# Performance work log

Hardware: AMD Instinct MI355X
Metric: run time of the kernel (lower is better)

Reference implementation:

```python
import jax, jax.numpy as jnp
import numpy as np
import math

# Config mirroring init_kwargs / input_specs
BATCH, N, D_IN, RANK = 8, 2048, 256, 64
TAU = 1.0
TOPK = 32
EDGE_DROPOUT = 0.1
EPS = 1e-6


def setup_inputs() -> dict:
    key = jax.random.key(0)
    k1, k2, k3 = jax.random.split(key, 3)
    X = jax.random.normal(k1, (BATCH, N, D_IN), dtype=jnp.float32)
    W = jax.random.normal(k2, (D_IN, RANK), dtype=jnp.float32) / math.sqrt(D_IN)
    # b_init='identity_perturbed': identity plus small noise
    B = jnp.eye(RANK, dtype=jnp.float32) + 0.01 * jax.random.normal(k3, (RANK, RANK), dtype=jnp.float32)
    return {"X": X, "W": W, "B": B}


def _zero_diag(A):
    n = A.shape[-1]
    return A * (1.0 - jnp.eye(n, dtype=A.dtype))


def _row_normalize(A):
    denom = jnp.clip(jnp.sum(A, axis=-1, keepdims=True), EPS, None)
    return A / denom


def reference(X, W, B):
    # FDG: low-rank node embedding R, bilinear scores S, softmax adjacency A
    R = jnp.einsum('bnd,dr->bnr', X, W)                       # [B, N, rank]
    S = jnp.einsum('bnr,rk,bmk->bnm', R, B, R) / jnp.asarray(math.sqrt(RANK), R.dtype)  # [B, N, N]
    A = jax.nn.softmax(S / TAU, axis=-1)

    # topk_sparsify_adjacency (mask=None)
    scores = _zero_diag(A)
    k = max(1, min(TOPK, N - 1))
    vals, idx = jax.lax.top_k(scores, k)                      # [B, N, k]
    bI = jnp.arange(BATCH)[:, None, None]
    nI = jnp.arange(N)[None, :, None]
    sparse = jnp.zeros_like(scores).at[bI, nI, idx].set(vals)
    A = _row_normalize(sparse)

    # edge_dropout_adjacency (training=True)
    keep_prob = 1.0 - EDGE_DROPOUT
    keep = (jax.random.uniform(jax.random.key(42), A.shape) <= keep_prob).astype(A.dtype)
    A = _zero_diag(A) * keep / max(keep_prob, 1e-6)
    A = _row_normalize(A)
    return (A, S, R)
```

## Files before the change

### kernel.cpp

```cpp
#include <hip/hip_runtime.h>
#include <math.h>

#define BATCH 8
#define NN 2048
#define DIN 256
#define RANK 64
#define TOPKK 32

static constexpr size_t A_ELEMS = (size_t)BATCH * NN * NN;
static constexpr size_t S_OFF   = A_ELEMS;
static constexpr size_t R_OFF   = 2 * A_ELEMS;

#define NEG_INF (-__builtin_inff())

__device__ __forceinline__ unsigned rotl32(unsigned x, int d) {
  return (x << d) | (x >> (32 - d));
}

__device__ unsigned threefry_bits(unsigned flat) {
  const unsigned ks0 = 0u, ks1 = 42u, ks2 = 0u ^ 42u ^ 0x1BD11BDAu;
  unsigned x0 = 0u + ks0;
  unsigned x1 = flat + ks1;
#define TF_ROUND(r) { x0 += x1; x1 = rotl32(x1, r); x1 ^= x0; }
  TF_ROUND(13) TF_ROUND(15) TF_ROUND(26) TF_ROUND(6)
  x0 += ks1; x1 += ks2 + 1u;
  TF_ROUND(17) TF_ROUND(29) TF_ROUND(16) TF_ROUND(24)
  x0 += ks2; x1 += ks0 + 2u;
  TF_ROUND(13) TF_ROUND(15) TF_ROUND(26) TF_ROUND(6)
  x0 += ks0; x1 += ks1 + 3u;
  TF_ROUND(17) TF_ROUND(29) TF_ROUND(16) TF_ROUND(24)
  x0 += ks1; x1 += ks2 + 4u;
  TF_ROUND(13) TF_ROUND(15) TF_ROUND(26) TF_ROUND(6)
  x0 += ks2; x1 += ks0 + 5u;
#undef TF_ROUND
  return x0 ^ x1;
}

__device__ __forceinline__ unsigned long long make_key(float v, int col) {
  unsigned u = __float_as_uint(v);
  u = (u & 0x80000000u) ? ~u : (u | 0x80000000u);
  return ((unsigned long long)u << 32) | (unsigned)(~col);
}

__global__ __launch_bounds__(256) void rt_kernel(const float* __restrict__ X,
                                                 const float* __restrict__ W,
                                                 const float* __restrict__ Bm,
                                                 float* __restrict__ out) {
  __shared__ float Xs[32][256];
  __shared__ float Bs[64][64];
  __shared__ float Rs[32][64];
  const int t = threadIdx.x;
  const int blk = blockIdx.x;
  const int b  = blk >> 6;
  const int rb = blk & 63;
  const float* Xb = X + ((size_t)b * NN + (size_t)rb * 32) * DIN;

#pragma unroll
  for (int it = 0; it < 8; ++it) {
    int flat = it * 1024 + t * 4;
    float4 f = *(const float4*)(Xb + flat);
    *(float4*)&Xs[flat >> 8][flat & 255] = f;
  }
#pragma unroll
  for (int it = 0; it < 4; ++it) {
    int flat = it * 1024 + t * 4;
    float4 f = *(const float4*)(Bm + flat);
    *(float4*)&Bs[flat >> 6][flat & 63] = f;
  }
  __syncthreads();

  const int j = t & 63, rg = t >> 6;
  float acc[8] = {0.f, 0.f, 0.f, 0.f, 0.f, 0.f, 0.f, 0.f};
  for (int k = 0; k < DIN; k += 4) {
    float w0 = W[(k + 0) * RANK + j];
    float w1 = W[(k + 1) * RANK + j];
    float w2 = W[(k + 2) * RANK + j];
    float w3 = W[(k + 3) * RANK + j];
#pragma unroll
    for (int ii = 0; ii < 8; ++ii) {
      float4 xv = *(const float4*)&Xs[rg * 8 + ii][k];
      acc[ii] += xv.x * w0 + xv.y * w1 + xv.z * w2 + xv.w * w3;
    }
  }
  const size_t grow0 = (size_t)b * NN + (size_t)rb * 32;
  float* Rout = out + R_OFF + grow0 * RANK;
#pragma unroll
  for (int ii = 0; ii < 8; ++ii) {
    Rout[(size_t)(rg * 8 + ii) * RANK + j] = acc[ii];
    Rs[rg * 8 + ii][j] = acc[ii];
  }
  __syncthreads();

  float acc2[8] = {0.f, 0.f, 0.f, 0.f, 0.f, 0.f, 0.f, 0.f};
  for (int r = 0; r < RANK; r += 4) {
    float b0 = Bs[r + 0][j];
    float b1 = Bs[r + 1][j];
    float b2 = Bs[r + 2][j];
    float b3 = Bs[r + 3][j];
#pragma unroll
    for (int ii = 0; ii < 8; ++ii) {
      float4 rv = *(const float4*)&Rs[rg * 8 + ii][r];
      acc2[ii] += rv.x * b0 + rv.y * b1 + rv.z * b2 + rv.w * b3;
    }
  }
  float* Tout = out + grow0 * RANK;
#pragma unroll
  for (int ii = 0; ii < 8; ++ii)
    Tout[(size_t)(rg * 8 + ii) * RANK + j] = acc2[ii] * 0.125f;
}

__global__ __launch_bounds__(256) void s_kernel(float* __restrict__ out) {
  __shared__ float Ts[64][68];
  __shared__ float Rs[64][68];
  const int t = threadIdx.x;
  const int bx = blockIdx.x;
  const int by = blockIdx.y;
  const int bz = blockIdx.z;
  const float* Tg = out + ((size_t)bz * NN + (size_t)by * 64) * RANK;
  const float* Rg = out + R_OFF + ((size_t)bz * NN + (size_t)bx * 64) * RANK;

#pragma unroll
  for (int it = 0; it < 4; ++it) {
    int flat = it * 1024 + t * 4;
    int r = flat >> 6, c = flat & 63;
    *(float4*)&Ts[r][c] = *(const float4*)(Tg + flat);
    *(float4*)&Rs[r][c] = *(const float4*)(Rg + flat);
  }
  __syncthreads();

  const int tx = t & 15, ty = t >> 4;
  float acc[4][4];
#pragma unroll
  for (int ii = 0; ii < 4; ++ii)
#pragma unroll
    for (int jj = 0; jj < 4; ++jj) acc[ii][jj] = 0.f;

  for (int k = 0; k < 64; k += 4) {
    float4 a[4], bb[4];
#pragma unroll
    for (int ii = 0; ii < 4; ++ii) a[ii] = *(const float4*)&Ts[ty + 16 * ii][k];
#pragma unroll
    for (int jj = 0; jj < 4; ++jj) bb[jj] = *(const float4*)&Rs[tx + 16 * jj][k];
#pragma unroll
    for (int ii = 0; ii < 4; ++ii)
#pragma unroll
      for (int jj = 0; jj < 4; ++jj)
        acc[ii][jj] += a[ii].x * bb[jj].x + a[ii].y * bb[jj].y +
                       a[ii].z * bb[jj].z + a[ii].w * bb[jj].w;
  }

  float* Sb = out + S_OFF + (size_t)bz * NN * NN;
#pragma unroll
  for (int ii = 0; ii < 4; ++ii) {
    int n = by * 64 + ty + 16 * ii;
#pragma unroll
    for (int jj = 0; jj < 4; ++jj) {
      int m = bx * 64 + tx + 16 * jj;
      Sb[(size_t)n * NN + m] = acc[ii][jj];
    }
  }
}

__global__ __launch_bounds__(64) void topk_kernel(const float* __restrict__ Sg,
                                                  float* __restrict__ A) {
  __shared__ float rowbuf[NN];
  __shared__ unsigned long long keys[64];
  __shared__ int cnt;
  const int lane = threadIdx.x;
  const int wave = blockIdx.x;
  const int n = wave & (NN - 1);

  const float* row = Sg + (size_t)wave * NN;
  float v[32];
#pragma unroll
  for (int jj = 0; jj < 8; ++jj) {
    float4 f = *(const float4*)(row + jj * 256 + lane * 4);
    v[jj * 4 + 0] = f.x; v[jj * 4 + 1] = f.y;
    v[jj * 4 + 2] = f.z; v[jj * 4 + 3] = f.w;
  }

  float s = 0.f, ss = 0.f;
#pragma unroll
  for (int jj = 0; jj < 32; ++jj) { s += v[jj]; ss = fmaf(v[jj], v[jj], ss); }
#pragma unroll
  for (int off = 1; off < 64; off <<= 1) {
    s  += __shfl_xor(s, off, 64);
    ss += __shfl_xor(ss, off, 64);
  }
  const float mu = s * (1.f / 2048.f);
  const float sigma = sqrtf(fmaxf(ss * (1.f / 2048.f) - mu * mu, 1e-12f));

  {
    int d = n - lane * 4;
    if (d >= 0 && d < NN && (d & 255) < 4)
      v[((d >> 8) << 2) | (d & 3)] = NEG_INF;
  }

  float tau = mu + 2.0641f * sigma;
  float lo_b = -3.0e38f, hi_b = 3.0e38f;
  float step = sigma + 1e-20f;
  bool found = false;
  for (int it = 0; it < 40; ++it) {
    int cl = 0;
#pragma unroll
    for (int jj = 0; jj < 32; ++jj) cl += (v[jj] > tau) ? 1 : 0;
#pragma unroll
    for (int off = 1; off < 64; off <<= 1) cl += __shfl_xor(cl, off, 64);
    if (cl >= TOPKK && cl <= 64) { found = true; break; }
    if (cl > 64) lo_b = fmaxf(lo_b, tau); else hi_b = fminf(hi_b, tau);
    float tn = 0.f; bool ok = false;
    if (it < 6) {
      float p = fminf(fmaxf((float)cl, 1.f) * (1.f / 2048.f), 0.5f);
      float tt = sqrtf(-2.f * logf(p));
      float zc = tt - (2.30753f + 0.27061f * tt) /
                      (1.f + tt * (0.99229f + 0.04481f * tt));
      zc = fmaxf(zc, 0.05f);
      tn = mu + 2.0641f * ((tau - mu) / zc);
      ok = (tn > lo_b && tn < hi_b);
    }
    if (!ok) {
      if (lo_b > -1.0e38f && hi_b < 1.0e38f) tn = 0.5f * lo_b + 0.5f * hi_b;
      else if (cl > 64) { tn = tau + step; step *= 2.f; }
      else             { tn = tau - step; step *= 2.f; }
    }
    tau = tn;
  }

  if (lane == 0) cnt = 0;
  __syncthreads();

  if (found) {
#pragma unroll
    for (int jj = 0; jj < 32; ++jj) {
      if (v[jj] > tau) {
        int col = ((jj >> 2) << 8) + lane * 4 + (jj & 3);
        int pos = atomicAdd(&cnt, 1);
        if (pos < 64) keys[pos] = make_key(v[jj], col);
      }
    }
  } else {
    unsigned alive = 0xFFFFFFFFu;
    if (lane == 0) cnt = TOPKK;
    for (int it = 0; it < TOPKK; ++it) {
      unsigned long long best = 0ull;
#pragma unroll
      for (int jj = 0; jj < 32; ++jj) {
        if ((alive >> jj) & 1u) {
          int col = ((jj >> 2) << 8) + lane * 4 + (jj & 3);
          unsigned long long k = make_key(v[jj], col);
          if (k > best) best = k;
        }
      }
      unsigned long long b2 = best;
#pragma unroll
      for (int off = 1; off < 64; off <<= 1) {
        unsigned long long o = __shfl_xor(b2, off, 64);
        if (o > b2) b2 = o;
      }
      if (lane == 0) keys[it] = b2;
      if (best == b2) {
#pragma unroll
        for (int jj = 0; jj < 32; ++jj) {
          int col = ((jj >> 2) << 8) + lane * 4 + (jj & 3);
          if (make_key(v[jj], col) == b2) alive &= ~(1u << jj);
        }
      }
    }
  }
  __syncthreads();

  const int cn = min(cnt, 64);
  unsigned long long key = (lane < cn) ? keys[lane] : 0ull;

#pragma unroll
  for (int k = 2; k <= 64; k <<= 1) {
#pragma unroll
    for (int j = k >> 1; j >= 1; j >>= 1) {
      unsigned long long o = __shfl_xor(key, j, 64);
      bool lower = (lane & j) == 0;
      bool desc  = (lane & k) == 0;
      bool takeMax = (lower == desc);
      bool kgo = key > o;
      key = (takeMax == kgo) ? key : o;
    }
  }

  float val; int col;
  {
    unsigned hi = (unsigned)(key >> 32);
    unsigned ub = (hi & 0x80000000u) ? (hi ^ 0x80000000u) : ~hi;
    val = __uint_as_float(ub);
    col = (int)(~(unsigned)key) & (NN - 1);
  }

  float m = __shfl(val, 0, 64);
  float e = (lane < TOPKK) ? expf(val - m) : 0.f;
  float s1 = e;
#pragma unroll
  for (int off = 1; off < 64; off <<= 1) s1 += __shfl_xor(s1, off, 64);
  float a1 = e / fmaxf(s1, 1e-6f);

  float a2 = 0.f;
  if (lane < TOPKK) {
    unsigned flat = (unsigned)wave * 2048u + (unsigned)col;
    unsigned bits = threefry_bits(flat);
    float u = __uint_as_float((bits >> 9) | 0x3f800000u) - 1.0f;
    if (u <= 0.9f) a2 = a1 * (1.f / 0.9f);
  }
  float s2 = a2;
#pragma unroll
  for (int off = 1; off < 64; off <<= 1) s2 += __shfl_xor(s2, off, 64);
  float av = a2 / fmaxf(s2, 1e-6f);

#pragma unroll
  for (int jj = 0; jj < 8; ++jj)
    *(float4*)&rowbuf[jj * 256 + lane * 4] = make_float4(0.f, 0.f, 0.f, 0.f);
  __syncthreads();
  if (lane < TOPKK) rowbuf[col] = av;
  __syncthreads();
  float* Arow = A + (size_t)wave * NN;
#pragma unroll
  for (int jj = 0; jj < 8; ++jj)
    *(float4*)(Arow + jj * 256 + lane * 4) = *(float4*)&rowbuf[jj * 256 + lane * 4];
}

extern "C" void kernel_launch(void* const* d_in, const int* in_sizes, int n_in,
                              void* d_out, int out_size, void* d_ws, size_t ws_size,
                              hipStream_t stream) {
  const float* X  = (const float*)d_in[0];
  const float* W  = (const float*)d_in[1];
  const float* Bm = (const float*)d_in[2];
  float* out = (float*)d_out;

  hipLaunchKernelGGL(rt_kernel, dim3(512), dim3(256), 0, stream, X, W, Bm, out);
  hipLaunchKernelGGL(s_kernel, dim3(32, 32, 8), dim3(256), 0, stream, out);
  hipLaunchKernelGGL(topk_kernel, dim3(16384), dim3(64), 0, stream, out + S_OFF, out);
}
```

Baseline: 163.7 us.

## Fuse S computation with threshold candidate extraction using analytic row statistics

Computes per-batch Gram matrix R^T R and column sums of R, then derives each row's mean and variance of S analytically to set a top-k threshold before S is formed. The S GEMM kernel now also emits candidate keys above that threshold into a workspace, so the top-k pass mostly sorts a short candidate list instead of rereading and iteratively thresholding the full S row. Rows whose candidate count falls outside the accepted range fall back to the old full-row search. This adds workspace traffic, atomics and two small reduction kernels. The fused kernel uses only 256 blocks of 512 threads, which risks underfilling the GPU.

After: 207.9 us. 27.0% more time.

```diff
diff --git a/kernel.cpp b/kernel.cpp
--- a/kernel.cpp
+++ b/kernel.cpp
@@ -6,10 +6,18 @@
 #define DIN 256
 #define RANK 64
 #define TOPKK 32
+#define CANDMAX 96
 
 static constexpr size_t A_ELEMS = (size_t)BATCH * NN * NN;
 static constexpr size_t S_OFF   = A_ELEMS;
 static constexpr size_t R_OFF   = 2 * A_ELEMS;
+static constexpr size_t NROWS   = (size_t)BATCH * NN;
+
+static constexpr size_t G_OFF      = 0;
+static constexpr size_t U_OFF      = 32768;
+static constexpr size_t GP_OFF     = 33280;
+static constexpr size_t CNT_OFF_F  = GP_OFF + 64 * 4160;
+static constexpr size_t CAND_OFF_F = CNT_OFF_F + NROWS;
 
 #define NEG_INF (-__builtin_inff())
 
@@ -42,6 +50,28 @@
   return ((unsigned long long)u << 32) | (unsigned)(~col);
 }
 
+__device__ __forceinline__ void decode_key(unsigned long long key, float& val, int& col) {
+  unsigned hi = (unsigned)(key >> 32);
+  unsigned ub = (hi & 0x80000000u) ? (hi ^ 0x80000000u) : ~hi;
+  val = __uint_as_float(ub);
+  col = (int)(~(unsigned)key) & (NN - 1);
+}
+
+__device__ __forceinline__ void bitonic64_desc(unsigned long long& key, int lane) {
+#pragma unroll
+  for (int k = 2; k <= 64; k <<= 1) {
+#pragma unroll
+    for (int j = k >> 1; j >= 1; j >>= 1) {
+      unsigned long long o = __shfl_xor(key, j, 64);
+      bool lower = (lane & j) == 0;
+      bool desc  = (lane & k) == 0;
+      bool takeMax = (lower == desc);
+      bool kgo = key > o;
+      key = (takeMax == kgo) ? key : o;
+    }
+  }
+}
+
 __global__ __launch_bounds__(256) void rt_kernel(const float* __restrict__ X,
                                                  const float* __restrict__ W,
                                                  const float* __restrict__ Bm,
@@ -58,14 +88,12 @@
 #pragma unroll
   for (int it = 0; it < 8; ++it) {
     int flat = it * 1024 + t * 4;
-    float4 f = *(const float4*)(Xb + flat);
-    *(float4*)&Xs[flat >> 8][flat & 255] = f;
+    *(float4*)&Xs[flat >> 8][flat & 255] = *(const float4*)(Xb + flat);
   }
 #pragma unroll
   for (int it = 0; it < 4; ++it) {
     int flat = it * 1024 + t * 4;
-    float4 f = *(const float4*)(Bm + flat);
-    *(float4*)&Bs[flat >> 6][flat & 63] = f;
+    *(float4*)&Bs[flat >> 6][flat & 63] = *(const float4*)(Bm + flat);
   }
   __syncthreads();
 
@@ -109,189 +137,317 @@
     Tout[(size_t)(rg * 8 + ii) * RANK + j] = acc2[ii] * 0.125f;
 }
 
-__global__ __launch_bounds__(256) void s_kernel(float* __restrict__ out) {
-  __shared__ float Ts[64][68];
-  __shared__ float Rs[64][68];
+__global__ __launch_bounds__(256) void ga_kernel(const float* __restrict__ out,
+                                                 float* __restrict__ ws) {
+  __shared__ float Rl[128][68];
   const int t = threadIdx.x;
-  const int bx = blockIdx.x;
-  const int by = blockIdx.y;
-  const int bz = blockIdx.z;
-  const float* Tg = out + ((size_t)bz * NN + (size_t)by * 64) * RANK;
-  const float* Rg = out + R_OFF + ((size_t)bz * NN + (size_t)bx * 64) * RANK;
-
-#pragma unroll
-  for (int it = 0; it < 4; ++it) {
-    int flat = it * 1024 + t * 4;
-    int r = flat >> 6, c = flat & 63;
-    *(float4*)&Ts[r][c] = *(const float4*)(Tg + flat);
-    *(float4*)&Rs[r][c] = *(const float4*)(Rg + flat);
-  }
-  __syncthreads();
-
-  const int tx = t & 15, ty = t >> 4;
+  const int b = blockIdx.x >> 3, chunk = blockIdx.x & 7;
+  const float* Rb = out + R_OFF + ((size_t)b * NN + (size_t)chunk * 256) * RANK;
+  const int i0 = (t >> 4) * 4, j0 = (t & 15) * 4;
   float acc[4][4];
 #pragma unroll
-  for (int ii = 0; ii < 4; ++ii)
-#pragma unroll
-    for (int jj = 0; jj < 4; ++jj) acc[ii][jj] = 0.f;
-
-  for (int k = 0; k < 64; k += 4) {
-    float4 a[4], bb[4];
-#pragma unroll
-    for (int ii = 0; ii < 4; ++ii) a[ii] = *(const float4*)&Ts[ty + 16 * ii][k];
-#pragma unroll
-    for (int jj = 0; jj < 4; ++jj) bb[jj] = *(const float4*)&Rs[tx + 16 * jj][k];
-#pragma unroll
-    for (int ii = 0; ii < 4; ++ii)
-#pragma unroll
-      for (int jj = 0; jj < 4; ++jj)
-        acc[ii][jj] += a[ii].x * bb[jj].x + a[ii].y * bb[jj].y +
-                       a[ii].z * bb[jj].z + a[ii].w * bb[jj].w;
-  }
-
-  float* Sb = out + S_OFF + (size_t)bz * NN * NN;
-#pragma unroll
-  for (int ii = 0; ii < 4; ++ii) {
-    int n = by * 64 + ty + 16 * ii;
-#pragma unroll
-    for (int jj = 0; jj < 4; ++jj) {
-      int m = bx * 64 + tx + 16 * jj;
-      Sb[(size_t)n * NN + m] = acc[ii][jj];
-    }
-  }
-}
-
-__global__ __launch_bounds__(64) void topk_kernel(const float* __restrict__ Sg,
-                                                  float* __restrict__ A) {
-  __shared__ float rowbuf[NN];
-  __shared__ unsigned long long keys[64];
-  __shared__ int cnt;
-  const int lane = threadIdx.x;
-  const int wave = blockIdx.x;
-  const int n = wave & (NN - 1);
-
-  const float* row = Sg + (size_t)wave * NN;
-  float v[32];
-#pragma unroll
-  for (int jj = 0; jj < 8; ++jj) {
-    float4 f = *(const float4*)(row + jj * 256 + lane * 4);
-    v[jj * 4 + 0] = f.x; v[jj * 4 + 1] = f.y;
-    v[jj * 4 + 2] = f.z; v[jj * 4 + 3] = f.w;
-  }
-
-  float s = 0.f, ss = 0.f;
-#pragma unroll
-  for (int jj = 0; jj < 32; ++jj) { s += v[jj]; ss = fmaf(v[jj], v[jj], ss); }
-#pragma unroll
-  for (int off = 1; off < 64; off <<= 1) {
-    s  += __shfl_xor(s, off, 64);
-    ss += __shfl_xor(ss, off, 64);
-  }
-  const float mu = s * (1.f / 2048.f);
-  const float sigma = sqrtf(fmaxf(ss * (1.f / 2048.f) - mu * mu, 1e-12f));
+  for (int a = 0; a < 4; ++a)
+#pragma unroll
+    for (int c = 0; c < 4; ++c) acc[a][c] = 0.f;
+  float uacc = 0.f;
+
+  for (int s2 = 0; s2 < 2; ++s2) {
+    const float* src = Rb + (size_t)s2 * 128 * RANK;
+#pragma unroll
+    for (int it = 0; it < 8; ++it) {
+      int flat = it * 1024 + t * 4;
+      *(float4*)&Rl[flat >> 6][flat & 63] = *(const float4*)(src + flat);
+    }
+    __syncthreads();
+    for (int r = 0; r < 128; ++r) {
+      float4 a = *(const float4*)&Rl[r][i0];
+      float4 bb = *(const float4*)&Rl[r][j0];
+      acc[0][0] = fmaf(a.x, bb.x, acc[0][0]); acc[0][1] = fmaf(a.x, bb.y, acc[0][1]);
+      acc[0][2] = fmaf(a.x, bb.z, acc[0][2]); acc[0][3] = fmaf(a.x, bb.w, acc[0][3]);
+      acc[1][0] = fmaf(a.y, bb.x, acc[1][0]); acc[1][1] = fmaf(a.y, bb.y, acc[1][1]);
+      acc[1][2] = fmaf(a.y, bb.z, acc[1][2]); acc[1][3] = fmaf(a.y, bb.w, acc[1][3]);
+      acc[2][0] = fmaf(a.z, bb.x, acc[2][0]); acc[2][1] = fmaf(a.z, bb.y, acc[2][1]);
+      acc[2][2] = fmaf(a.z, bb.z, acc[2][2]); acc[2][3] = fmaf(a.z, bb.w, acc[2][3]);
+      acc[3][0] = fmaf(a.w, bb.x, acc[3][0]); acc[3][1] = fmaf(a.w, bb.y, acc[3][1]);
+      acc[3][2] = fmaf(a.w, bb.z, acc[3][2]); acc[3][3] = fmaf(a.w, bb.w, acc[3][3]);
+    }
+    if (t < 64) {
+      for (int r = 0; r < 128; ++r) uacc += Rl[r][t];
+    }
+    __syncthreads();
+  }
+  float* dst = ws + GP_OFF + (size_t)blockIdx.x * 4160;
+#pragma unroll
+  for (int a = 0; a < 4; ++a) {
+    float4 f = make_float4(acc[a][0], acc[a][1], acc[a][2], acc[a][3]);
+    *(float4*)&dst[(i0 + a) * 64 + j0] = f;
+  }
+  if (t < 64) dst[4096 + t] = uacc;
+}
+
+__global__ __launch_bounds__(256) void gb_kernel(float* __restrict__ ws) {
+  const int b = blockIdx.x, t = threadIdx.x;
+  for (int idx = t; idx < 4160; idx += 256) {
+    float s = 0.f;
+    for (int c = 0; c < 8; ++c)
+      s += ws[GP_OFF + (size_t)(b * 8 + c) * 4160 + idx];
+    if (idx < 4096) ws[G_OFF + (size_t)b * 4096 + idx] = s;
+    else            ws[U_OFF + (size_t)b * 64 + (idx - 4096)] = s;
+  }
+}
+
+__global__ __launch_bounds__(512) void fuseda_kernel(float* __restrict__ out,
+                                                     float* __restrict__ ws) {
+  __shared__ float Tk[64][64];
+  __shared__ float Rk[64][128];
+  __shared__ float u_l[64];
+  __shared__ float tau_l[64];
+  __shared__ int   cnt_l[64];
+
+  const int t = threadIdx.x;
+  const int bid = blockIdx.x;
+  const int b = bid >> 5, p = bid & 31;
+  const int n0 = p * 64;
+  const size_t g0 = (size_t)b * NN + n0;
+
+  const float* Tsrc = out + g0 * RANK;
+  const float* Rsrc = out + R_OFF + (size_t)b * NN * RANK;
+  float* Sbase = out + S_OFF + (size_t)b * NN * NN;
+  unsigned long long* cand = (unsigned long long*)(ws + CAND_OFF_F);
+  int* cnt_ws = (int*)(ws + CNT_OFF_F);
+
+#pragma unroll
+  for (int it = 0; it < 2; ++it) {
+    int flat = it * 2048 + t * 4;
+    int r = flat >> 6, k0 = flat & 63;
+    float4 f = *(const float4*)(Tsrc + flat);
+    Tk[k0 + 0][r] = f.x; Tk[k0 + 1][r] = f.y;
+    Tk[k0 + 2][r] = f.z; Tk[k0 + 3][r] = f.w;
+  }
+  if (t < 64) { u_l[t] = ws[U_OFF + (size_t)b * 64 + t]; cnt_l[t] = 0; }
+  __syncthreads();
 
   {
-    int d = n - lane * 4;
-    if (d >= 0 && d < NN && (d & 255) < 4)
-      v[((d >> 8) << 2) | (d & 3)] = NEG_INF;
-  }
-
-  float tau = mu + 2.0641f * sigma;
-  float lo_b = -3.0e38f, hi_b = 3.0e38f;
-  float step = sigma + 1e-20f;
-  bool found = false;
-  for (int it = 0; it < 40; ++it) {
-    int cl = 0;
-#pragma unroll
-    for (int jj = 0; jj < 32; ++jj) cl += (v[jj] > tau) ? 1 : 0;
-#pragma unroll
-    for (int off = 1; off < 64; off <<= 1) cl += __shfl_xor(cl, off, 64);
-    if (cl >= TOPKK && cl <= 64) { found = true; break; }
-    if (cl > 64) lo_b = fmaxf(lo_b, tau); else hi_b = fminf(hi_b, tau);
-    float tn = 0.f; bool ok = false;
-    if (it < 6) {
-      float p = fminf(fmaxf((float)cl, 1.f) * (1.f / 2048.f), 0.5f);
-      float tt = sqrtf(-2.f * logf(p));
-      float zc = tt - (2.30753f + 0.27061f * tt) /
-                      (1.f + tt * (0.99229f + 0.04481f * tt));
-      zc = fmaxf(zc, 0.05f);
-      tn = mu + 2.0641f * ((tau - mu) / zc);
-      ok = (tn > lo_b && tn < hi_b);
-    }
-    if (!ok) {
-      if (lo_b > -1.0e38f && hi_b < 1.0e38f) tn = 0.5f * lo_b + 0.5f * hi_b;
-      else if (cl > 64) { tn = tau + step; step *= 2.f; }
-      else             { tn = tau - step; step *= 2.f; }
-    }
-    tau = tn;
-  }
-
-  if (lane == 0) cnt = 0;
-  __syncthreads();
-
-  if (found) {
-#pragma unroll
-    for (int jj = 0; jj < 32; ++jj) {
-      if (v[jj] > tau) {
-        int col = ((jj >> 2) << 8) + lane * 4 + (jj & 3);
-        int pos = atomicAdd(&cnt, 1);
-        if (pos < 64) keys[pos] = make_key(v[jj], col);
-      }
+    const int wave = t >> 6, lane = t & 63;
+    const float* Gb = ws + G_OFF + (size_t)b * 4096;
+    for (int q = 0; q < 8; ++q) {
+      int row = wave * 8 + q;
+      float gj = 0.f, mua = 0.f;
+      for (int k = 0; k < 64; ++k) {
+        float tk = Tk[k][row];
+        gj  = fmaf(tk, Gb[k * 64 + lane], gj);
+        mua = fmaf(tk, u_l[k], mua);
+      }
+      float tj = Tk[lane][row];
+      float qq = gj * tj;
+#pragma unroll
+      for (int off = 1; off < 64; off <<= 1) qq += __shfl_xor(qq, off, 64);
+      float ms = qq * (1.f / 2048.f);
+      float mu = mua * (1.f / 2048.f);
+      float sigma = sqrtf(fmaxf(ms - mu * mu, 1e-12f));
+      if (lane == 0) tau_l[row] = mu + 1.8627f * sigma;
+    }
+  }
+  __syncthreads();
+
+  const int tx = t & 31, ty = t >> 5;
+  float taur[4];
+#pragma unroll
+  for (int i = 0; i < 4; ++i) taur[i] = tau_l[ty * 4 + i];
+
+  float4 pf[4];
+#define STAGE_ISSUE(tile) {                                                  \
+  _Pragma("unroll")                                                          \
+  for (int it = 0; it < 4; ++it) {                                           \
+    int flat = it * 2048 + t * 4;                                            \
+    int c = flat >> 6, k0 = flat & 63;                                       \
+    pf[it] = *(const float4*)(Rsrc + (size_t)((tile) * 128 + c) * RANK + k0);\
+  } }
+#define STAGE_WRITE() {                                                      \
+  _Pragma("unroll")                                                          \
+  for (int it = 0; it < 4; ++it) {                                           \
+    int flat = it * 2048 + t * 4;                                            \
+    int c = flat >> 6, k0 = flat & 63;                                       \
+    Rk[k0 + 0][c] = pf[it].x; Rk[k0 + 1][c] = pf[it].y;                      \
+    Rk[k0 + 2][c] = pf[it].z; Rk[k0 + 3][c] = pf[it].w;                      \
+  } }
+
+  STAGE_ISSUE(0); STAGE_WRITE();
+  __syncthreads();
+
+  for (int tile = 0; tile < 16; ++tile) {
+    if (tile < 15) STAGE_ISSUE(tile + 1);
+
+    float4 accv[4];
+#pragma unroll
+    for (int i = 0; i < 4; ++i) accv[i] = make_float4(0.f, 0.f, 0.f, 0.f);
+    for (int k = 0; k < 64; ++k) {
+      float4 a  = *(const float4*)&Tk[k][ty * 4];
+      float4 bb = *(const float4*)&Rk[k][tx * 4];
+      accv[0].x = fmaf(a.x, bb.x, accv[0].x); accv[0].y = fmaf(a.x, bb.y, accv[0].y);
+      accv[0].z = fmaf(a.x, bb.z, accv[0].z); accv[0].w = fmaf(a.x, bb.w, accv[0].w);
+      accv[1].x = fmaf(a.y, bb.x, accv[1].x); accv[1].y = fmaf(a.y, bb.y, accv[1].y);
+      accv[1].z = fmaf(a.y, bb.z, accv[1].z); accv[1].w = fmaf(a.y, bb.w, accv[1].w);
+      accv[2].x = fmaf(a.z, bb.x, accv[2].x); accv[2].y = fmaf(a.z, bb.y, accv[2].y);
+      accv[2].z = fmaf(a.z, bb.z, accv[2].z); accv[2].w = fmaf(a.z, bb.w, accv[2].w);
+      accv[3].x = fmaf(a.w, bb.x, accv[3].x); accv[3].y = fmaf(a.w, bb.y, accv[3].y);
+      accv[3].z = fmaf(a.w, bb.z, accv[3].z); accv[3].w = fmaf(a.w, bb.w, accv[3].w);
+    }
+
+#pragma unroll
+    for (int i = 0; i < 4; ++i) {
+      int rl = ty * 4 + i;
+      int grow = n0 + rl;
+      *(float4*)(Sbase + (size_t)grow * NN + tile * 128 + tx * 4) = accv[i];
+      const float vv[4] = {accv[i].x, accv[i].y, accv[i].z, accv[i].w};
+#pragma unroll
+      for (int jj = 0; jj < 4; ++jj) {
+        int col = tile * 128 + tx * 4 + jj;
+        float v = vv[jj];
+        if (col != grow && v > taur[i]) {
+          int pos = atomicAdd(&cnt_l[rl], 1);
+          if (pos < CANDMAX)
+            cand[(g0 + rl) * CANDMAX + pos] = make_key(v, col);
+        }
+      }
+    }
+    __syncthreads();
+    if (tile < 15) { STAGE_WRITE(); }
+    __syncthreads();
+  }
+#undef STAGE_ISSUE
+#undef STAGE_WRITE
+
+  if (t < 64) cnt_ws[g0 + t] = cnt_l[t];
+}
+
+__global__ __launch_bounds__(256) void fusedb_kernel(float* __restrict__ out,
+                                                     const float* __restrict__ ws) {
+  __shared__ unsigned long long wbuf[4][64];
+  __shared__ int fcnt[4];
+  __shared__ float rowbuf[4][2048];
+  const int t = threadIdx.x;
+  const int wv = t >> 6, lane = t & 63;
+  const int g = blockIdx.x * 4 + wv;
+  const int n = g & (NN - 1);
+
+  const unsigned long long* crow =
+      (const unsigned long long*)(ws + CAND_OFF_F) + (size_t)g * CANDMAX;
+  const int c = ((const int*)(ws + CNT_OFF_F))[g];
+
+  unsigned long long key = 0ull;
+  if (c >= TOPKK && c <= CANDMAX) {
+    if (c <= 64) {
+      key = (lane < c) ? crow[lane] : 0ull;
+      bitonic64_desc(key, lane);
+    } else {
+      key = crow[lane];
+      bitonic64_desc(key, lane);
+      if (lane >= 32) { int idx = 64 + (lane - 32); key = (idx < c) ? crow[idx] : 0ull; }
+      bitonic64_desc(key, lane);
     }
   } else {
-    unsigned alive = 0xFFFFFFFFu;
-    if (lane == 0) cnt = TOPKK;
-    for (int it = 0; it < TOPKK; ++it) {
-      unsigned long long best = 0ull;
+    const float* row = out + S_OFF + (size_t)g * NN;
+    float v[32];
+#pragma unroll
+    for (int jj = 0; jj < 8; ++jj) {
+      float4 f = *(const float4*)(row + jj * 256 + lane * 4);
+      v[jj * 4 + 0] = f.x; v[jj * 4 + 1] = f.y;
+      v[jj * 4 + 2] = f.z; v[jj * 4 + 3] = f.w;
+    }
+    float s = 0.f, ss = 0.f;
+#pragma unroll
+    for (int jj = 0; jj < 32; ++jj) { s += v[jj]; ss = fmaf(v[jj], v[jj], ss); }
+#pragma unroll
+    for (int off = 1; off < 64; off <<= 1) {
+      s += __shfl_xor(s, off, 64); ss += __shfl_xor(ss, off, 64);
+    }
+    const float mu = s * (1.f / 2048.f);
+    const float sigma = sqrtf(fmaxf(ss * (1.f / 2048.f) - mu * mu, 1e-12f));
+    {
+      int d = n - lane * 4;
+      if (d >= 0 && d < NN && (d & 255) < 4) v[((d >> 8) << 2) | (d & 3)] = NEG_INF;
+    }
+    float tau = mu + 2.0641f * sigma;
+    float lo_b = -3.0e38f, hi_b = 3.0e38f;
+    float step = sigma + 1e-20f;
+    bool found = false;
+    for (int it = 0; it < 40; ++it) {
+      int cl = 0;
+#pragma unroll
+      for (int jj = 0; jj < 32; ++jj) cl += (v[jj] > tau) ? 1 : 0;
+#pragma unroll
+      for (int off = 1; off < 64; off <<= 1) cl += __shfl_xor(cl, off, 64);
+      if (cl >= TOPKK && cl <= 64) { found = true; break; }
+      if (cl > 64) lo_b = fmaxf(lo_b, tau); else hi_b = fminf(hi_b, tau);
+      float tn = 0.f; bool ok = false;
+      if (it < 6) {
+        float pp = fminf(fmaxf((float)cl, 1.f) * (1.f / 2048.f), 0.5f);
+        float tt = sqrtf(-2.f * logf(pp));
+        float zc = tt - (2.30753f + 0.27061f * tt) /
+                        (1.f + tt * (0.99229f + 0.04481f * tt));
+        zc = fmaxf(zc, 0.05f);
+        tn = mu + 2.0641f * ((tau - mu) / zc);
+        ok = (tn > lo_b && tn < hi_b);
+      }
+      if (!ok) {
+        if (lo_b > -1.0e38f && hi_b < 1.0e38f) tn = 0.5f * lo_b + 0.5f * hi_b;
+        else if (cl > 64) { tn = tau + step; step *= 2.f; }
+        else              { tn = tau - step; step *= 2.f; }
+      }
+      tau = tn;
+    }
+    if (found) {
+      if (lane == 0) fcnt[wv] = 0;
+      int mycnt = 0;
 #pragma unroll
       for (int jj = 0; jj < 32; ++jj) {
-        if ((alive >> jj) & 1u) {
+        if (v[jj] > tau) {
           int col = ((jj >> 2) << 8) + lane * 4 + (jj & 3);
-          unsigned long long k = make_key(v[jj], col);
-          if (k > best) best = k;
+          int pos = atomicAdd(&fcnt[wv], 1);
+          wbuf[wv][pos] = make_key(v[jj], col);
+          ++mycnt;
         }
       }
-      unsigned long long b2 = best;
-#pragma unroll
-      for (int off = 1; off < 64; off <<= 1) {
-        unsigned long long o = __shfl_xor(b2, off, 64);
-        if (o > b2) b2 = o;
-      }
-      if (lane == 0) keys[it] = b2;
-      if (best == b2) {
+      int fc = mycnt;
+#pragma unroll
+      for (int off = 1; off < 64; off <<= 1) fc += __shfl_xor(fc, off, 64);
+      key = (lane < fc) ? wbuf[wv][lane] : 0ull;
+      bitonic64_desc(key, lane);
+    } else {
+      unsigned alive = 0xFFFFFFFFu;
+      unsigned long long keysel = 0ull;
+      for (int it = 0; it < TOPKK; ++it) {
+        unsigned long long best = 0ull;
 #pragma unroll
         for (int jj = 0; jj < 32; ++jj) {
-          int col = ((jj >> 2) << 8) + lane * 4 + (jj & 3);
-          if (make_key(v[jj], col) == b2) alive &= ~(1u << jj);
+          if ((alive >> jj) & 1u) {
+            int col = ((jj >> 2) << 8) + lane * 4 + (jj & 3);
+            unsigned long long kk = make_key(v[jj], col);
+            if (kk > best) best = kk;
+          }
         }
-      }
-    }
-  }
-  __syncthreads();
-
-  const int cn = min(cnt, 64);
-  unsigned long long key = (lane < cn) ? keys[lane] : 0ull;
-
-#pragma unroll
-  for (int k = 2; k <= 64; k <<= 1) {
-#pragma unroll
-    for (int j = k >> 1; j >= 1; j >>= 1) {
-      unsigned long long o = __shfl_xor(key, j, 64);
-      bool lower = (lane & j) == 0;
-      bool desc  = (lane & k) == 0;
-      bool takeMax = (lower == desc);
-      bool kgo = key > o;
-      key = (takeMax == kgo) ? key : o;
+        unsigned long long b2 = best;
+#pragma unroll
+        for (int off = 1; off < 64; off <<= 1) {
+          unsigned long long o = __shfl_xor(b2, off, 64);
+          if (o > b2) b2 = o;
+        }
+        if (lane == it) keysel = b2;
+        if (best == b2) {
+#pragma unroll
+          for (int jj = 0; jj < 32; ++jj) {
+            int col = ((jj >> 2) << 8) + lane * 4 + (jj & 3);
+            if (make_key(v[jj], col) == b2) alive &= ~(1u << jj);
+          }
+        }
+      }
+      key = keysel;
     }
   }
 
   float val; int col;
-  {
-    unsigned hi = (unsigned)(key >> 32);
-    unsigned ub = (hi & 0x80000000u) ? (hi ^ 0x80000000u) : ~hi;
-    val = __uint_as_float(ub);
-    col = (int)(~(unsigned)key) & (NN - 1);
-  }
+  decode_key(key, val, col);
 
   float m = __shfl(val, 0, 64);
   float e = (lane < TOPKK) ? expf(val - m) : 0.f;
@@ -302,7 +458,7 @@
 
   float a2 = 0.f;
   if (lane < TOPKK) {
-    unsigned flat = (unsigned)wave * 2048u + (unsigned)col;
+    unsigned flat = (unsigned)g * 2048u + (unsigned)col;
     unsigned bits = threefry_bits(flat);
     float u = __uint_as_float((bits >> 9) | 0x3f800000u) - 1.0f;
     if (u <= 0.9f) a2 = a1 * (1.f / 0.9f);
@@ -314,14 +470,14 @@
 
 #pragma unroll
   for (int jj = 0; jj < 8; ++jj)
-    *(float4*)&rowbuf[jj * 256 + lane * 4] = make_float4(0.f, 0.f, 0.f, 0.f);
-  __syncthreads();
-  if (lane < TOPKK) rowbuf[col] = av;
-  __syncthreads();
-  float* Arow = A + (size_t)wave * NN;
+    *(float4*)&rowbuf[wv][jj * 256 + lane * 4] = make_float4(0.f, 0.f, 0.f, 0.f);
+  __syncthreads();
+  if (lane < TOPKK) rowbuf[wv][col] = av;
+  __syncthreads();
+  float* Arow = out + (size_t)g * NN;
 #pragma unroll
   for (int jj = 0; jj < 8; ++jj)
-    *(float4*)(Arow + jj * 256 + lane * 4) = *(float4*)&rowbuf[jj * 256 + lane * 4];
+    *(float4*)(Arow + jj * 256 + lane * 4) = *(float4*)&rowbuf[wv][jj * 256 + lane * 4];
 }
 
 extern "C" void kernel_launch(void* const* d_in, const int* in_sizes, int n_in,
@@ -331,8 +487,11 @@
   const float* W  = (const float*)d_in[1];
   const float* Bm = (const float*)d_in[2];
   float* out = (float*)d_out;
+  float* ws  = (float*)d_ws;
 
   hipLaunchKernelGGL(rt_kernel, dim3(512), dim3(256), 0, stream, X, W, Bm, out);
-  hipLaunchKernelGGL(s_kernel, dim3(32, 32, 8), dim3(256), 0, stream, out);
-  hipLaunchKernelGGL(topk_kernel, dim3(16384), dim3(64), 0, stream, out + S_OFF, out);
-}
+  hipLaunchKernelGGL(ga_kernel, dim3(64), dim3(256), 0, stream, out, ws);
+  hipLaunchKernelGGL(gb_kernel, dim3(8), dim3(256), 0, stream, ws);
+  hipLaunchKernelGGL(fuseda_kernel, dim3(256), dim3(512), 0, stream, out, ws);
+  hipLaunchKernelGGL(fusedb_kernel, dim3(4096), dim3(256), 0, stream, out, ws);
+}
```
